# Kernel tuning notes

Measured on AMD Instinct MI355X. Metric: run time of the kernel, lower is better.

Reference implementation:

```python
import jax, jax.numpy as jnp
import numpy as np

NUM_HEADS = 32
ROPE_BASE = 10000.0
MASK_NEG = -66504.0  # from (1 - tril) * -66504.0 in the source


def _rotate_half(x):
    d = x.shape[-1] // 2
    return jnp.concatenate([-x[..., d:], x[..., :d]], axis=-1)


def setup_inputs() -> dict:
    key = jax.random.key(0)
    k1, k2, k3, k4 = jax.random.split(key, 4)
    S, B, E = 2048, 2, 2048
    return {
        "hidden_states": jax.random.normal(k1, (S, B, E), dtype=jnp.float32) * 0.02,
        "qkv_w": jax.random.normal(k2, (E, 3 * E), dtype=jnp.float32) * 0.02,
        "qkv_b": jax.random.normal(k3, (3 * E,), dtype=jnp.float32) * 0.02,
        "out_w": jax.random.normal(k4, (E, E), dtype=jnp.float32) * 0.02,
        "out_b": jnp.zeros((E,), dtype=jnp.float32),
    }


def reference(hidden_states, qkv_w, qkv_b, out_w, out_b):
    # seq-first prompt/prefill path of IPEXTransformerAtten
    S, B, E = hidden_states.shape
    H = NUM_HEADS
    D = E // H

    # fused QKV projection (mm_qkv_out)
    qkv = jnp.einsum('sbe,ef->sbf', hidden_states, qkv_w) + qkv_b  # [S,B,3E]
    q, k, v = jnp.split(qkv, 3, axis=-1)
    q = q.reshape(S, B, H, D)
    k = k.reshape(S, B, H, D)
    v = v.reshape(S, B, H, D)

    # rotary embedding (GPT-NeoX style, full head_dim)
    inv_freq = 1.0 / (ROPE_BASE ** (jnp.arange(0, D, 2, dtype=jnp.float32) / D))
    freqs = jnp.arange(S, dtype=jnp.float32)[:, None] * inv_freq  # [S, D/2]
    emb = jnp.concatenate([freqs, freqs], axis=-1)  # [S, D]
    cos = jnp.cos(emb)[:, None, None, :].astype(hidden_states.dtype)
    sin = jnp.sin(emb)[:, None, None, :].astype(hidden_states.dtype)
    q = q * cos + _rotate_half(q) * sin
    k = k * cos + _rotate_half(k) * sin

    # scaled dot-product attention with causal mask
    scale = 1.0 / jnp.sqrt(jnp.array(D, dtype=hidden_states.dtype))
    scores = jnp.einsum('sbhd,tbhd->bhst', q, k) * scale  # [B,H,S,S]
    causal = jnp.tril(jnp.ones((S, S), dtype=scores.dtype))
    scores = scores + (1.0 - causal) * MASK_NEG
    attn = jax.nn.softmax(scores, axis=-1)
    ctx = jnp.einsum('bhst,tbhd->sbhd', attn, v).reshape(S, B, E)

    # output projection
    return jnp.einsum('sbe,ef->sbf', ctx, out_w) + out_b
```

## Files before the change

### kernel.cpp

```cpp
#include <hip/hip_runtime.h>
#include <hip/hip_bf16.h>

#define S_LEN 2048
#define BATCH 2
#define EMB   2048
#define NH    32
#define HD    64
#define M_ROWS (S_LEN * BATCH)
#define QKV_N  (3 * EMB)

typedef short bf16x8 __attribute__((ext_vector_type(8)));
typedef float f32x4  __attribute__((ext_vector_type(4)));

__device__ __forceinline__ unsigned short f2bf(float f) {
  unsigned int u = __float_as_uint(f);
  u += 0x7fffu + ((u >> 16) & 1u);
  return (unsigned short)(u >> 16);
}
__device__ __forceinline__ float bf2f(unsigned short h) {
  return __uint_as_float(((unsigned int)h) << 16);
}
__device__ __forceinline__ void async_copy16(const void* g, void* lds_d) {
  __builtin_amdgcn_global_load_lds(
      (const __attribute__((address_space(1))) void*)g,
      (__attribute__((address_space(3))) void*)lds_d, 16, 0, 0);
}

#if __has_builtin(__builtin_amdgcn_exp2f)
#define EXP2F(x) __builtin_amdgcn_exp2f(x)
#else
#define EXP2F(x) __expf((x) * 0.6931471805599453f)
#endif


__global__ __launch_bounds__(256) void cast_to_bf16(
    const float* __restrict__ in, unsigned short* __restrict__ out, int n4) {
  int i = blockIdx.x * 256 + threadIdx.x;
  if (i >= n4) return;
  float4 v = reinterpret_cast<const float4*>(in)[i];
  ushort4 o;
  o.x = f2bf(v.x); o.y = f2bf(v.y); o.z = f2bf(v.z); o.w = f2bf(v.w);
  reinterpret_cast<ushort4*>(out)[i] = o;
}

__global__ __launch_bounds__(256) void transpose_cast(
    const float* __restrict__ in, unsigned short* __restrict__ out, int R, int C) {
  __shared__ unsigned short t[64][65];
  const int bc = blockIdx.x * 64, br = blockIdx.y * 64;
  const int tx = threadIdx.x & 63, ty = threadIdx.x >> 6;
  #pragma unroll
  for (int rr = ty; rr < 64; rr += 4)
    t[rr][tx] = f2bf(in[(size_t)(br + rr) * C + bc + tx]);
  __syncthreads();
  #pragma unroll
  for (int rr = ty; rr < 64; rr += 4)
    out[(size_t)(bc + rr) * R + br + tx] = t[tx][rr];
}


constexpr int TILE_SH = 24576;
constexpr int GEMM_LDS_BYTES = 3 * TILE_SH * 2;

__global__ __launch_bounds__(512, 2) void gemm_qkv(
    const unsigned short* __restrict__ A,
    const unsigned short* __restrict__ Wt,
    const float* __restrict__ bias,
    unsigned short* __restrict__ Qo,
    unsigned short* __restrict__ Ko,
    unsigned short* __restrict__ Vo) {
  extern __shared__ unsigned short lds[];
  const int tid = threadIdx.x;
  const int n0 = blockIdx.x * 128;
  const int m0 = blockIdx.y * 256;
  const int wave = tid >> 6, lane = tid & 63;
  const int wm = (wave >> 1) * 64, wn = (wave & 1) * 64;
  const int lm = lane & 15, lq = lane >> 4;
  const int K = 2048;
  const int NT = K / 64;

  const int srow = tid >> 3;
  const int gch  = (tid & 7) ^ (srow & 7);
  const unsigned short* Ab = A  + (size_t)(m0 + srow) * K + gch * 8;
  const unsigned short* Bb = Wt + (size_t)(n0 + srow) * K + gch * 8;

  auto stA = [&](int bufi, int k0, int rep) {
    async_copy16(Ab + (size_t)rep * 64 * K + k0,
                 lds + (size_t)bufi * TILE_SH + ((size_t)rep * 512 + tid) * 8);
  };
  auto stB = [&](int bufi, int k0, int rep) {
    async_copy16(Bb + (size_t)rep * 64 * K + k0,
                 lds + (size_t)bufi * TILE_SH + 16384 + ((size_t)rep * 512 + tid) * 8);
  };

  f32x4 acc[4][4] = {};

  stA(0, 0, 0); stA(0, 0, 1); stA(0, 0, 2); stA(0, 0, 3); stB(0, 0, 0); stB(0, 0, 1);
  stA(1, 64, 0); stA(1, 64, 1); stA(1, 64, 2); stA(1, 64, 3); stB(1, 64, 0); stB(1, 64, 1);
  asm volatile("s_waitcnt vmcnt(6)" ::: "memory");
  __builtin_amdgcn_s_barrier();

  int cur = 0;
  for (int t = 0; t < NT; t++) {
    const unsigned short* Abuf = lds + (size_t)cur * TILE_SH;
    const unsigned short* Bbuf = Abuf + 16384;
    const int pb = (cur >= 1) ? cur - 1 : 2;
    const int pk = (t + 2) * 64;
    const bool pre = (t + 2) < NT;

    bf16x8 b[4][2], a[2][2];
    #pragma unroll
    for (int j = 0; j < 4; j++) {
      const int R = wn + j * 16 + lm;
      #pragma unroll
      for (int ks = 0; ks < 2; ks++)
        b[j][ks] = *reinterpret_cast<const bf16x8*>(
            Bbuf + (size_t)R * 64 + (((ks * 4 + lq) ^ (R & 7)) * 8));
    }
    #pragma unroll
    for (int i = 0; i < 2; i++) {
      const int R = wm + i * 16 + lm;
      #pragma unroll
      for (int ks = 0; ks < 2; ks++)
        a[i][ks] = *reinterpret_cast<const bf16x8*>(
            Abuf + (size_t)R * 64 + (((ks * 4 + lq) ^ (R & 7)) * 8));
    }
    if (pre) { stA(pb, pk, 0); stA(pb, pk, 1); stB(pb, pk, 0); }
    __builtin_amdgcn_s_barrier();
    asm volatile("s_waitcnt lgkmcnt(0)" ::: "memory");
    __builtin_amdgcn_s_setprio(1);
    #pragma unroll
    for (int ks = 0; ks < 2; ks++)
      #pragma unroll
      for (int i = 0; i < 2; i++)
        #pragma unroll
        for (int j = 0; j < 4; j++)
          acc[i][j] = __builtin_amdgcn_mfma_f32_16x16x32_bf16(a[i][ks], b[j][ks], acc[i][j], 0, 0, 0);
    __builtin_amdgcn_s_setprio(0);
    __builtin_amdgcn_s_barrier();

    #pragma unroll
    for (int i = 0; i < 2; i++) {
      const int R = wm + (i + 2) * 16 + lm;
      #pragma unroll
      for (int ks = 0; ks < 2; ks++)
        a[i][ks] = *reinterpret_cast<const bf16x8*>(
            Abuf + (size_t)R * 64 + (((ks * 4 + lq) ^ (R & 7)) * 8));
    }
    if (pre) { stA(pb, pk, 2); stA(pb, pk, 3); stB(pb, pk, 1); }
    __builtin_amdgcn_s_barrier();
    asm volatile("s_waitcnt lgkmcnt(0)" ::: "memory");
    __builtin_amdgcn_s_setprio(1);
    #pragma unroll
    for (int ks = 0; ks < 2; ks++)
      #pragma unroll
      for (int i = 0; i < 2; i++)
        #pragma unroll
        for (int j = 0; j < 4; j++)
          acc[i + 2][j] = __builtin_amdgcn_mfma_f32_16x16x32_bf16(a[i][ks], b[j][ks], acc[i + 2][j], 0, 0, 0);
    __builtin_amdgcn_s_setprio(0);
    if (t + 1 < NT) {
      if (pre) asm volatile("s_waitcnt vmcnt(6)" ::: "memory");
      else     asm volatile("s_waitcnt vmcnt(0)" ::: "memory");
      __builtin_amdgcn_s_barrier();
    }
    cur = (cur == 2) ? 0 : cur + 1;
  }

  const int which = n0 >> 11;
  unsigned short* dst = (which == 0) ? Qo : (which == 1) ? Ko : Vo;
  float bv[4];
  #pragma unroll
  for (int j = 0; j < 4; j++) bv[j] = bias[n0 + wn + j * 16 + lm];

  if (which < 2) {
    #pragma unroll
    for (int j = 0; j < 2; j++) {
      const int n = n0 + wn + j * 16 + lm;
      const int e = n & (EMB - 1), h = e >> 6, d = e & 63;
      const float invf = EXP2F((float)d * -0.4152410118609203f);
      #pragma unroll
      for (int i = 0; i < 4; i++) {
        #pragma unroll
        for (int r = 0; r < 4; r++) {
          const int m = m0 + wm + i * 16 + lq * 4 + r;
          const int s = m >> 1, b = m & 1;
          const float v1 = acc[i][j][r]     + bv[j];
          const float v2 = acc[i][j + 2][r] + bv[j + 2];
          float sn, cs;
          __sincosf((float)s * invf, &sn, &cs);
          const size_t base = (((size_t)b * NH + h) * S_LEN + s) * HD + d;
          dst[base]      = f2bf(v1 * cs - v2 * sn);
          dst[base + 32] = f2bf(v2 * cs + v1 * sn);
        }
      }
    }
  } else {
    #pragma unroll
    for (int j = 0; j < 4; j++) {
      const int n = n0 + wn + j * 16 + lm;
      const int e = n & (EMB - 1), h = e >> 6, d = e & 63;
      #pragma unroll
      for (int i = 0; i < 4; i++) {
        #pragma unroll
        for (int r = 0; r < 4; r++) {
          const int m = m0 + wm + i * 16 + lq * 4 + r;
          const int s = m >> 1, b = m & 1;
          dst[(((size_t)b * NH + h) * S_LEN + s) * HD + d] = f2bf(acc[i][j][r] + bv[j]);
        }
      }
    }
  }
}


__global__ __launch_bounds__(256) void transpose_v(
    const unsigned short* __restrict__ V, unsigned short* __restrict__ VT) {
  __shared__ unsigned short t[64][65];
  const int bh = blockIdx.y;
  const int s0 = blockIdx.x * 64;
  const int tx = threadIdx.x & 63, ty = threadIdx.x >> 6;
  const unsigned short* src = V + ((size_t)bh * S_LEN + s0) * HD;
  #pragma unroll
  for (int r = ty; r < 64; r += 4)
    t[r][tx] = src[(size_t)r * HD + tx];
  __syncthreads();
  unsigned short* dst = VT + (size_t)bh * HD * S_LEN + s0;
  #pragma unroll
  for (int r = ty; r < 64; r += 4)
    dst[(size_t)r * S_LEN + tx] = t[tx][r];
}


__global__ __launch_bounds__(256) void attn_kernel(
    const unsigned short* __restrict__ Q,
    const unsigned short* __restrict__ K,
    const unsigned short* __restrict__ VT,
    unsigned short* __restrict__ ctx) {
  const int bh = blockIdx.x;
  const int p  = blockIdx.y;
  const int tid = threadIdx.x;
  const int wave = tid >> 6, lane = tid & 63;
  const int lm = lane & 15, lq = lane >> 4;
  const int b = bh >> 5, h = bh & 31;
  const char* Qb8 = (const char*)(Q  + (size_t)bh * S_LEN * HD);
  const char* Kb8 = (const char*)(K  + (size_t)bh * S_LEN * HD);
  const char* Vb8 = (const char*)(VT + (size_t)bh * HD * S_LEN);

  __shared__ __align__(16) unsigned short Ks[2][2][64][32];
  __shared__ __align__(16) unsigned short Pbuf[4][32][72];
  unsigned short* Pw = &Pbuf[wave][0][0];

  const float C = 0.18033688011112042f;
  const int q0A = p * 128, q0B = (15 - p) * 128;
  const int r0A = q0A + wave * 32, r0B = q0B + wave * 32;
  const int nt = (q0B >> 6) + 2;

  const int srw = tid >> 2, sc16 = (tid & 3) * 16;

  bf16x8 qf[2][2][2];
  #pragma unroll
  for (int s = 0; s < 2; s++) {
    const int rr = (s == 0) ? r0A : r0B;
    #pragma unroll
    for (int i = 0; i < 2; i++)
      #pragma unroll
      for (int ks = 0; ks < 2; ks++)
        qf[s][i][ks] = *reinterpret_cast<const bf16x8*>(
            Qb8 + (size_t)(rr + i*16 + lm) * 128 + ks*64 + lq*16);
  }

  f32x4 O[2][2][4] = {};
  float l[2][2][4] = {};

  {
    char* kd = (char*)&Ks[0][0][0][0];
    async_copy16(Kb8 + (size_t)srw * 128      + sc16, kd        + tid*16);
    async_copy16(Kb8 + (size_t)srw * 128 + 64 + sc16, kd + 4096 + tid*16);
  }
  __syncthreads();

  for (int t = 0; t < nt; t++) {
    const int t0 = t * 64;
    const int buf = t & 1;

    if (t + 1 < nt) {
      const int t1 = t0 + 64;
      char* kd = (char*)&Ks[buf ^ 1][0][0][0];
      async_copy16(Kb8 + (size_t)(t1 + srw) * 128      + sc16, kd        + tid*16);
      async_copy16(Kb8 + (size_t)(t1 + srw) * 128 + 64 + sc16, kd + 4096 + tid*16);
    }

    const char* KsB = (const char*)&Ks[buf][0][0][0];

    #pragma unroll
    for (int s = 0; s < 2; s++) {
      const int rr = (s == 0) ? r0A : r0B;
      if (t0 <= rr + 31) {
        const bool clean = (t0 + 63 <= rr);
        const int jmax  = clean ? 4 : ((rr == t0) ? 2 : 4);
        const int kslim = clean ? 2 : ((rr == t0) ? 1 : 2);
        const int srow_c = rr + lq * 4;

        f32x4 sc[2][4] = {};
        #pragma unroll
        for (int ks = 0; ks < 2; ks++) {
          bf16x8 kf[4];
          #pragma unroll
          for (int j = 0; j < 4; j++)
            if (j < jmax)
              kf[j] = *reinterpret_cast<const bf16x8*>(
                  KsB + ks*4096 + (j*16 + lm)*64 + lq*16);
          #pragma unroll
          for (int i = 0; i < 2; i++)
            #pragma unroll
            for (int j = 0; j < 4; j++)
              if (j < jmax)
                sc[i][j] = __builtin_amdgcn_mfma_f32_16x16x32_bf16(
                    qf[s][i][ks], kf[j], sc[i][j], 0, 0, 0);
        }

        if (clean) {
          #pragma unroll
          for (int i = 0; i < 2; i++)
            #pragma unroll
            for (int j = 0; j < 4; j++)
              #pragma unroll
              for (int r = 0; r < 4; r++) {
                const float pe = EXP2F(sc[i][j][r] * C);
                l[s][i][r] += pe;
                Pw[(i*16 + lq*4 + r) * 72 + j*16 + lm] = f2bf(pe);
              }
        } else {
          #pragma unroll
          for (int i = 0; i < 2; i++)
            #pragma unroll
            for (int j = 0; j < 4; j++)
              if (j < jmax)
                #pragma unroll
                for (int r = 0; r < 4; r++) {
                  const int srow = srow_c + i*16 + r;
                  const int tcol = t0 + j*16 + lm;
                  const float pe = (tcol <= srow) ? EXP2F(sc[i][j][r] * C) : 0.0f;
                  l[s][i][r] += pe;
                  Pw[(i*16 + lq*4 + r) * 72 + j*16 + lm] = f2bf(pe);
                }
        }

        #pragma unroll
        for (int ks = 0; ks < 2; ks++) {
          if (ks < kslim) {
            bf16x8 pf[2], vf[4];
            #pragma unroll
            for (int i = 0; i < 2; i++)
              pf[i] = *reinterpret_cast<const bf16x8*>(Pw + (i*16 + lm)*72 + ks*32 + lq*8);
            #pragma unroll
            for (int j = 0; j < 4; j++)
              vf[j] = *reinterpret_cast<const bf16x8*>(
                  Vb8 + (size_t)(j*16 + lm) * 4096 + t0*2 + ks*64 + lq*16);
            #pragma unroll
            for (int i = 0; i < 2; i++)
              #pragma unroll
              for (int j = 0; j < 4; j++)
                O[s][i][j] = __builtin_amdgcn_mfma_f32_16x16x32_bf16(
                    pf[i], vf[j], O[s][i][j], 0, 0, 0);
          }
        }
      }
    }
    __syncthreads();
  }

  #pragma unroll
  for (int s = 0; s < 2; s++) {
    const int rr = (s == 0) ? r0A : r0B;
    #pragma unroll
    for (int i = 0; i < 2; i++) {
      #pragma unroll
      for (int r = 0; r < 4; r++) {
        float sum = l[s][i][r];
        sum += __shfl_xor(sum, 1, 64);
        sum += __shfl_xor(sum, 2, 64);
        sum += __shfl_xor(sum, 4, 64);
        sum += __shfl_xor(sum, 8, 64);
        const float inv = 1.0f / sum;
        const int srow = rr + lq*4 + i*16 + r;
        #pragma unroll
        for (int j = 0; j < 4; j++) {
          const int d = j*16 + lm;
          ctx[((size_t)srow * BATCH + b) * EMB + h*HD + d] = f2bf(O[s][i][j][r] * inv);
        }
      }
    }
  }
}


__global__ __launch_bounds__(512, 2) void gemm_out(
    const unsigned short* __restrict__ A,
    const unsigned short* __restrict__ Wt,
    const float* __restrict__ bias,
    float* __restrict__ out) {
  extern __shared__ unsigned short lds[];
  const int tid = threadIdx.x;
  const int n0 = blockIdx.x * 128;
  const int m0 = blockIdx.y * 256;
  const int wave = tid >> 6, lane = tid & 63;
  const int wm = (wave >> 1) * 64, wn = (wave & 1) * 64;
  const int lm = lane & 15, lq = lane >> 4;
  const int K = 2048;
  const int NT = K / 64;

  const int srow = tid >> 3;
  const int gch  = (tid & 7) ^ (srow & 7);
  const unsigned short* Ab = A  + (size_t)(m0 + srow) * K + gch * 8;
  const unsigned short* Bb = Wt + (size_t)(n0 + srow) * K + gch * 8;

  auto stA = [&](int bufi, int k0, int rep) {
    async_copy16(Ab + (size_t)rep * 64 * K + k0,
                 lds + (size_t)bufi * TILE_SH + ((size_t)rep * 512 + tid) * 8);
  };
  auto stB = [&](int bufi, int k0, int rep) {
    async_copy16(Bb + (size_t)rep * 64 * K + k0,
                 lds + (size_t)bufi * TILE_SH + 16384 + ((size_t)rep * 512 + tid) * 8);
  };

  f32x4 acc[4][4] = {};

  stA(0, 0, 0); stA(0, 0, 1); stA(0, 0, 2); stA(0, 0, 3); stB(0, 0, 0); stB(0, 0, 1);
  stA(1, 64, 0); stA(1, 64, 1); stA(1, 64, 2); stA(1, 64, 3); stB(1, 64, 0); stB(1, 64, 1);
  asm volatile("s_waitcnt vmcnt(6)" ::: "memory");
  __builtin_amdgcn_s_barrier();

  int cur = 0;
  for (int t = 0; t < NT; t++) {
    const unsigned short* Abuf = lds + (size_t)cur * TILE_SH;
    const unsigned short* Bbuf = Abuf + 16384;
    const int pb = (cur >= 1) ? cur - 1 : 2;
    const int pk = (t + 2) * 64;
    const bool pre = (t + 2) < NT;

    bf16x8 b[4][2], a[2][2];
    #pragma unroll
    for (int j = 0; j < 4; j++) {
      const int R = wn + j * 16 + lm;
      #pragma unroll
      for (int ks = 0; ks < 2; ks++)
        b[j][ks] = *reinterpret_cast<const bf16x8*>(
            Bbuf + (size_t)R * 64 + (((ks * 4 + lq) ^ (R & 7)) * 8));
    }
    #pragma unroll
    for (int i = 0; i < 2; i++) {
      const int R = wm + i * 16 + lm;
      #pragma unroll
      for (int ks = 0; ks < 2; ks++)
        a[i][ks] = *reinterpret_cast<const bf16x8*>(
            Abuf + (size_t)R * 64 + (((ks * 4 + lq) ^ (R & 7)) * 8));
    }
    if (pre) { stA(pb, pk, 0); stA(pb, pk, 1); stB(pb, pk, 0); }
    __builtin_amdgcn_s_barrier();
    asm volatile("s_waitcnt lgkmcnt(0)" ::: "memory");
    __builtin_amdgcn_s_setprio(1);
    #pragma unroll
    for (int ks = 0; ks < 2; ks++)
      #pragma unroll
      for (int i = 0; i < 2; i++)
        #pragma unroll
        for (int j = 0; j < 4; j++)
          acc[i][j] = __builtin_amdgcn_mfma_f32_16x16x32_bf16(a[i][ks], b[j][ks], acc[i][j], 0, 0, 0);
    __builtin_amdgcn_s_setprio(0);
    __builtin_amdgcn_s_barrier();

    #pragma unroll
    for (int i = 0; i < 2; i++) {
      const int R = wm + (i + 2) * 16 + lm;
      #pragma unroll
      for (int ks = 0; ks < 2; ks++)
        a[i][ks] = *reinterpret_cast<const bf16x8*>(
            Abuf + (size_t)R * 64 + (((ks * 4 + lq) ^ (R & 7)) * 8));
    }
    if (pre) { stA(pb, pk, 2); stA(pb, pk, 3); stB(pb, pk, 1); }
    __builtin_amdgcn_s_barrier();
    asm volatile("s_waitcnt lgkmcnt(0)" ::: "memory");
    __builtin_amdgcn_s_setprio(1);
    #pragma unroll
    for (int ks = 0; ks < 2; ks++)
      #pragma unroll
      for (int i = 0; i < 2; i++)
        #pragma unroll
        for (int j = 0; j < 4; j++)
          acc[i + 2][j] = __builtin_amdgcn_mfma_f32_16x16x32_bf16(a[i][ks], b[j][ks], acc[i + 2][j], 0, 0, 0);
    __builtin_amdgcn_s_setprio(0);
    if (t + 1 < NT) {
      if (pre) asm volatile("s_waitcnt vmcnt(6)" ::: "memory");
      else     asm volatile("s_waitcnt vmcnt(0)" ::: "memory");
      __builtin_amdgcn_s_barrier();
    }
    cur = (cur == 2) ? 0 : cur + 1;
  }

  #pragma unroll
  for (int j = 0; j < 4; j++) {
    const int n = n0 + wn + j * 16 + lm;
    const float bv = bias[n];
    #pragma unroll
    for (int i = 0; i < 4; i++) {
      #pragma unroll
      for (int r = 0; r < 4; r++) {
        const int m = m0 + wm + i * 16 + lq * 4 + r;
        out[(size_t)m * EMB + n] = acc[i][j][r] + bv;
      }
    }
  }
}


extern "C" void kernel_launch(void* const* d_in, const int* in_sizes, int n_in,
                              void* d_out, int out_size, void* d_ws, size_t ws_size,
                              hipStream_t stream) {
  const float* hidden = (const float*)d_in[0];
  const float* qkv_w  = (const float*)d_in[1];
  const float* qkv_b  = (const float*)d_in[2];
  const float* out_w  = (const float*)d_in[3];
  const float* out_b  = (const float*)d_in[4];
  float* out = (float*)d_out;

  static bool attr_set = false;
  if (!attr_set) {
    hipFuncSetAttribute(reinterpret_cast<const void*>(gemm_qkv),
                        hipFuncAttributeMaxDynamicSharedMemorySize, GEMM_LDS_BYTES);
    hipFuncSetAttribute(reinterpret_cast<const void*>(gemm_out),
                        hipFuncAttributeMaxDynamicSharedMemorySize, GEMM_LDS_BYTES);
    attr_set = true;
  }

  unsigned short* ws = (unsigned short*)d_ws;
  unsigned short* hbf   = ws;
  unsigned short* qkvwT = hbf   + (size_t)M_ROWS * EMB;
  unsigned short* outwT = qkvwT + (size_t)QKV_N * EMB;
  unsigned short* Qb    = outwT + (size_t)EMB * EMB;
  unsigned short* Kb    = Qb    + (size_t)64 * S_LEN * HD;
  unsigned short* Vb    = Kb    + (size_t)64 * S_LEN * HD;
  unsigned short* VTb   = Vb    + (size_t)64 * S_LEN * HD;
  unsigned short* ctx   = VTb   + (size_t)64 * S_LEN * HD;

  cast_to_bf16<<<(M_ROWS * EMB / 4) / 256, 256, 0, stream>>>(hidden, hbf, M_ROWS * EMB / 4);
  transpose_cast<<<dim3(QKV_N / 64, EMB / 64), 256, 0, stream>>>(qkv_w, qkvwT, EMB, QKV_N);
  transpose_cast<<<dim3(EMB / 64, EMB / 64), 256, 0, stream>>>(out_w, outwT, EMB, EMB);

  gemm_qkv<<<dim3(QKV_N / 128, M_ROWS / 256), 512, GEMM_LDS_BYTES, stream>>>(
      hbf, qkvwT, qkv_b, Qb, Kb, Vb);

  transpose_v<<<dim3(S_LEN / 64, 64), 256, 0, stream>>>(Vb, VTb);

  attn_kernel<<<dim3(64, 8), 256, 0, stream>>>(Qb, Kb, VTb, ctx);

  gemm_out<<<dim3(EMB / 128, M_ROWS / 256), 512, GEMM_LDS_BYTES, stream>>>(
      ctx, outwT, out_b, out);
}
```

Before: 399.9 us.

## Split attention query stripes across 8 waves and stage V tiles in LDS

The attention kernel moves from 256 to 512 threads. The two causal query stripes (A and B) are now handled by separate groups of 4 waves instead of each wave looping over both, which halves per-wave registers and raises wave-level parallelism. V tiles are now prefetched asynchronously into double-buffered LDS alongside K, rather than read directly from global memory inside the PV loop. The P buffer padding changes from 72 to 66. In exchange, each block uses more dynamic LDS, and waves in the short-stripe group sit idle while still joining the per-tile barriers.

```diff
diff --git a/kernel.cpp b/kernel.cpp
--- a/kernel.cpp
+++ b/kernel.cpp
@@ -231,51 +231,52 @@
 }
 
 
-__global__ __launch_bounds__(256) void attn_kernel(
+constexpr int ATTN_LDS_BYTES = 16384 + 16384 + 8 * 32 * 66 * 2;
+
+__global__ __launch_bounds__(512, 2) void attn_kernel(
     const unsigned short* __restrict__ Q,
     const unsigned short* __restrict__ K,
     const unsigned short* __restrict__ VT,
     unsigned short* __restrict__ ctx) {
+  extern __shared__ unsigned short lds[];
+  char* lds_c = (char*)lds;
   const int bh = blockIdx.x;
   const int p  = blockIdx.y;
   const int tid = threadIdx.x;
   const int wave = tid >> 6, lane = tid & 63;
   const int lm = lane & 15, lq = lane >> 4;
+  const int sgrp = wave >> 2;
+  const int w4 = wave & 3;
   const int b = bh >> 5, h = bh & 31;
   const char* Qb8 = (const char*)(Q  + (size_t)bh * S_LEN * HD);
   const char* Kb8 = (const char*)(K  + (size_t)bh * S_LEN * HD);
   const char* Vb8 = (const char*)(VT + (size_t)bh * HD * S_LEN);
 
-  __shared__ __align__(16) unsigned short Ks[2][2][64][32];
-  __shared__ __align__(16) unsigned short Pbuf[4][32][72];
-  unsigned short* Pw = &Pbuf[wave][0][0];
+  unsigned short* Pw = lds + 16384 + wave * 32 * 66;
 
   const float C = 0.18033688011112042f;
   const int q0A = p * 128, q0B = (15 - p) * 128;
-  const int r0A = q0A + wave * 32, r0B = q0B + wave * 32;
+  const int rr = (sgrp == 0 ? q0A : q0B) + w4 * 32;
   const int nt = (q0B >> 6) + 2;
 
-  const int srw = tid >> 2, sc16 = (tid & 3) * 16;
-
-  bf16x8 qf[2][2][2];
-  #pragma unroll
-  for (int s = 0; s < 2; s++) {
-    const int rr = (s == 0) ? r0A : r0B;
-    #pragma unroll
-    for (int i = 0; i < 2; i++)
-      #pragma unroll
-      for (int ks = 0; ks < 2; ks++)
-        qf[s][i][ks] = *reinterpret_cast<const bf16x8*>(
-            Qb8 + (size_t)(rr + i*16 + lm) * 128 + ks*64 + lq*16);
-  }
-
-  f32x4 O[2][2][4] = {};
-  float l[2][2][4] = {};
+  const int sthf = tid >> 8, strow = (tid >> 2) & 63, stch = tid & 3;
+
+  bf16x8 qf[2][2];
+  #pragma unroll
+  for (int i = 0; i < 2; i++)
+    #pragma unroll
+    for (int ks = 0; ks < 2; ks++)
+      qf[i][ks] = *reinterpret_cast<const bf16x8*>(
+          Qb8 + (size_t)(rr + i*16 + lm) * 128 + ks*64 + lq*16);
+
+  f32x4 O[2][4] = {};
+  float l[2][4] = {};
 
   {
-    char* kd = (char*)&Ks[0][0][0][0];
-    async_copy16(Kb8 + (size_t)srw * 128      + sc16, kd        + tid*16);
-    async_copy16(Kb8 + (size_t)srw * 128 + 64 + sc16, kd + 4096 + tid*16);
+    char* kd = lds_c;
+    char* vd = lds_c + 16384;
+    async_copy16(Kb8 + (size_t)strow * 128 + sthf * 64 + stch * 16, kd + tid * 16);
+    async_copy16(Vb8 + (size_t)strow * 4096 + sthf * 64 + stch * 16, vd + tid * 16);
   }
   __syncthreads();
 
@@ -285,110 +286,104 @@
 
     if (t + 1 < nt) {
       const int t1 = t0 + 64;
-      char* kd = (char*)&Ks[buf ^ 1][0][0][0];
-      async_copy16(Kb8 + (size_t)(t1 + srw) * 128      + sc16, kd        + tid*16);
-      async_copy16(Kb8 + (size_t)(t1 + srw) * 128 + 64 + sc16, kd + 4096 + tid*16);
-    }
-
-    const char* KsB = (const char*)&Ks[buf][0][0][0];
-
-    #pragma unroll
-    for (int s = 0; s < 2; s++) {
-      const int rr = (s == 0) ? r0A : r0B;
-      if (t0 <= rr + 31) {
-        const bool clean = (t0 + 63 <= rr);
-        const int jmax  = clean ? 4 : ((rr == t0) ? 2 : 4);
-        const int kslim = clean ? 2 : ((rr == t0) ? 1 : 2);
-        const int srow_c = rr + lq * 4;
-
-        f32x4 sc[2][4] = {};
-        #pragma unroll
-        for (int ks = 0; ks < 2; ks++) {
-          bf16x8 kf[4];
+      char* kd = lds_c + (buf ^ 1) * 8192;
+      char* vd = lds_c + 16384 + (buf ^ 1) * 8192;
+      async_copy16(Kb8 + (size_t)(t1 + strow) * 128 + sthf * 64 + stch * 16, kd + tid * 16);
+      async_copy16(Vb8 + (size_t)strow * 4096 + t1 * 2 + sthf * 64 + stch * 16, vd + tid * 16);
+    }
+
+    const char* KsB = lds_c + buf * 8192;
+    const char* VsB = lds_c + 16384 + buf * 8192;
+
+    if (t0 <= rr + 31) {
+      const bool clean = (t0 + 63 <= rr);
+      const int jmax  = clean ? 4 : ((rr == t0) ? 2 : 4);
+      const int kslim = clean ? 2 : ((rr == t0) ? 1 : 2);
+      const int srow_c = rr + lq * 4;
+
+      f32x4 sc[2][4] = {};
+      #pragma unroll
+      for (int ks = 0; ks < 2; ks++) {
+        bf16x8 kf[4];
+        #pragma unroll
+        for (int j = 0; j < 4; j++)
+          if (j < jmax)
+            kf[j] = *reinterpret_cast<const bf16x8*>(
+                KsB + ks*4096 + (j*16 + lm)*64 + lq*16);
+        #pragma unroll
+        for (int i = 0; i < 2; i++)
           #pragma unroll
           for (int j = 0; j < 4; j++)
             if (j < jmax)
-              kf[j] = *reinterpret_cast<const bf16x8*>(
-                  KsB + ks*4096 + (j*16 + lm)*64 + lq*16);
+              sc[i][j] = __builtin_amdgcn_mfma_f32_16x16x32_bf16(
+                  qf[i][ks], kf[j], sc[i][j], 0, 0, 0);
+      }
+
+      if (clean) {
+        #pragma unroll
+        for (int i = 0; i < 2; i++)
+          #pragma unroll
+          for (int j = 0; j < 4; j++)
+            #pragma unroll
+            for (int r = 0; r < 4; r++) {
+              const float pe = EXP2F(sc[i][j][r] * C);
+              l[i][r] += pe;
+              Pw[(i*16 + lq*4 + r) * 66 + j*16 + lm] = f2bf(pe);
+            }
+      } else {
+        #pragma unroll
+        for (int i = 0; i < 2; i++)
+          #pragma unroll
+          for (int j = 0; j < 4; j++)
+            if (j < jmax)
+              #pragma unroll
+              for (int r = 0; r < 4; r++) {
+                const int srow = srow_c + i*16 + r;
+                const int tcol = t0 + j*16 + lm;
+                const float pe = (tcol <= srow) ? EXP2F(sc[i][j][r] * C) : 0.0f;
+                l[i][r] += pe;
+                Pw[(i*16 + lq*4 + r) * 66 + j*16 + lm] = f2bf(pe);
+              }
+      }
+
+      #pragma unroll
+      for (int ks = 0; ks < 2; ks++) {
+        if (ks < kslim) {
+          bf16x8 pf[2], vf[4];
+          #pragma unroll
+          for (int i = 0; i < 2; i++)
+            pf[i] = *reinterpret_cast<const bf16x8*>(Pw + (i*16 + lm)*66 + ks*32 + lq*8);
+          #pragma unroll
+          for (int j = 0; j < 4; j++)
+            vf[j] = *reinterpret_cast<const bf16x8*>(
+                VsB + ks*4096 + (j*16 + lm)*64 + lq*16);
           #pragma unroll
           for (int i = 0; i < 2; i++)
             #pragma unroll
             for (int j = 0; j < 4; j++)
-              if (j < jmax)
-                sc[i][j] = __builtin_amdgcn_mfma_f32_16x16x32_bf16(
-                    qf[s][i][ks], kf[j], sc[i][j], 0, 0, 0);
+              O[i][j] = __builtin_amdgcn_mfma_f32_16x16x32_bf16(
+                  pf[i], vf[j], O[i][j], 0, 0, 0);
         }
-
-        if (clean) {
-          #pragma unroll
-          for (int i = 0; i < 2; i++)
-            #pragma unroll
-            for (int j = 0; j < 4; j++)
-              #pragma unroll
-              for (int r = 0; r < 4; r++) {
-                const float pe = EXP2F(sc[i][j][r] * C);
-                l[s][i][r] += pe;
-                Pw[(i*16 + lq*4 + r) * 72 + j*16 + lm] = f2bf(pe);
-              }
-        } else {
-          #pragma unroll
-          for (int i = 0; i < 2; i++)
-            #pragma unroll
-            for (int j = 0; j < 4; j++)
-              if (j < jmax)
-                #pragma unroll
-                for (int r = 0; r < 4; r++) {
-                  const int srow = srow_c + i*16 + r;
-                  const int tcol = t0 + j*16 + lm;
-                  const float pe = (tcol <= srow) ? EXP2F(sc[i][j][r] * C) : 0.0f;
-                  l[s][i][r] += pe;
-                  Pw[(i*16 + lq*4 + r) * 72 + j*16 + lm] = f2bf(pe);
-                }
-        }
-
-        #pragma unroll
-        for (int ks = 0; ks < 2; ks++) {
-          if (ks < kslim) {
-            bf16x8 pf[2], vf[4];
-            #pragma unroll
-            for (int i = 0; i < 2; i++)
-              pf[i] = *reinterpret_cast<const bf16x8*>(Pw + (i*16 + lm)*72 + ks*32 + lq*8);
-            #pragma unroll
-            for (int j = 0; j < 4; j++)
-              vf[j] = *reinterpret_cast<const bf16x8*>(
-                  Vb8 + (size_t)(j*16 + lm) * 4096 + t0*2 + ks*64 + lq*16);
-            #pragma unroll
-            for (int i = 0; i < 2; i++)
-              #pragma unroll
-              for (int j = 0; j < 4; j++)
-                O[s][i][j] = __builtin_amdgcn_mfma_f32_16x16x32_bf16(
-                    pf[i], vf[j], O[s][i][j], 0, 0, 0);
-          }
-        }
       }
     }
     __syncthreads();
   }
 
   #pragma unroll
-  for (int s = 0; s < 2; s++) {
-    const int rr = (s == 0) ? r0A : r0B;
-    #pragma unroll
-    for (int i = 0; i < 2; i++) {
-      #pragma unroll
-      for (int r = 0; r < 4; r++) {
-        float sum = l[s][i][r];
-        sum += __shfl_xor(sum, 1, 64);
-        sum += __shfl_xor(sum, 2, 64);
-        sum += __shfl_xor(sum, 4, 64);
-        sum += __shfl_xor(sum, 8, 64);
-        const float inv = 1.0f / sum;
-        const int srow = rr + lq*4 + i*16 + r;
-        #pragma unroll
-        for (int j = 0; j < 4; j++) {
-          const int d = j*16 + lm;
-          ctx[((size_t)srow * BATCH + b) * EMB + h*HD + d] = f2bf(O[s][i][j][r] * inv);
-        }
+  for (int i = 0; i < 2; i++) {
+    #pragma unroll
+    for (int r = 0; r < 4; r++) {
+      float sum = l[i][r];
+      sum += __shfl_xor(sum, 1, 64);
+      sum += __shfl_xor(sum, 2, 64);
+      sum += __shfl_xor(sum, 4, 64);
+      sum += __shfl_xor(sum, 8, 64);
+      const float inv = 1.0f / sum;
+      const int srow = rr + lq*4 + i*16 + r;
+      #pragma unroll
+      for (int j = 0; j < 4; j++) {
+        const int d = j*16 + lm;
+        ctx[((size_t)srow * BATCH + b) * EMB + h*HD + d] = f2bf(O[i][j][r] * inv);
       }
     }
   }
@@ -530,6 +525,8 @@
                         hipFuncAttributeMaxDynamicSharedMemorySize, GEMM_LDS_BYTES);
     hipFuncSetAttribute(reinterpret_cast<const void*>(gemm_out),
                         hipFuncAttributeMaxDynamicSharedMemorySize, GEMM_LDS_BYTES);
+    hipFuncSetAttribute(reinterpret_cast<const void*>(attn_kernel),
+                        hipFuncAttributeMaxDynamicSharedMemorySize, ATTN_LDS_BYTES);
     attr_set = true;
   }
 
@@ -552,7 +549,7 @@
 
   transpose_v<<<dim3(S_LEN / 64, 64), 256, 0, stream>>>(Vb, VTb);
 
-  attn_kernel<<<dim3(64, 8), 256, 0, stream>>>(Qb, Kb, VTb, ctx);
+  attn_kernel<<<dim3(64, 8), 512, ATTN_LDS_BYTES, stream>>>(Qb, Kb, VTb, ctx);
 
   gemm_out<<<dim3(EMB / 128, M_ROWS / 256), 512, GEMM_LDS_BYTES, stream>>>(
       ctx, outwT, out_b, out);
```

New measurement: 390.8 us. 1.02x faster.
